# Kernel optimization log

Hardware: AMD Instinct MI355X
Metric: run time of the kernel (lower is better)

The kernel has to match this reference:

```python
import jax, jax.numpy as jnp
import numpy as np

B, IN, OUT, E = 4096, 256, 256, 16


def setup_inputs() -> dict:
    key = jax.random.key(0)
    k1, k2, k3, k4, k5, k6 = jax.random.split(key, 6)
    return {
        "input": jax.random.normal(k1, (B, IN), dtype=jnp.float32),
        "route_index": jax.random.randint(k2, (B,), 0, E),
        "weight": jax.random.normal(k3, (E, OUT * IN), dtype=jnp.float32) * 0.02,
        "weight_fact": jax.random.normal(k4, (1, OUT * IN), dtype=jnp.float32) * 0.02,
        "bias": jax.random.normal(k5, (E, OUT), dtype=jnp.float32) * 0.02,
        "bias_fact": jax.random.normal(k6, (1, OUT), dtype=jnp.float32) * 0.02,
    }


def reference(input, route_index, weight, weight_fact, bias, bias_fact):
    b = input.shape[0]
    # per-token expert weight gather + shared factorized weight
    expert_weight = (weight[route_index] + weight_fact).reshape(b, OUT, IN)
    expert_bias = bias[route_index] + bias_fact  # [b, OUT]
    # batched matvec
    out = jnp.einsum("bmn,bn->bm", expert_weight, input) + expert_bias
    return out
```

## Files before the change

### kernel.cpp

```cpp
#include <hip/hip_runtime.h>


#define B_TOK 4096
#define IN_F 256
#define OUT_F 256
#define NEXP 16
#define WEL (OUT_F * IN_F)
#define NSB 16

typedef __attribute__((ext_vector_type(8))) short bhalf8;
typedef __attribute__((ext_vector_type(4))) float v4f;

__device__ __forceinline__ unsigned short f2bf(float f) {
    unsigned u = __float_as_uint(f);
    u += 0x7FFFu + ((u >> 16) & 1u);
    return (unsigned short)(u >> 16);
}

__device__ __forceinline__ bhalf8 cvt8(float4 a0, float4 a1) {
    bhalf8 v;
    v[0] = (short)f2bf(a0.x); v[1] = (short)f2bf(a0.y);
    v[2] = (short)f2bf(a0.z); v[3] = (short)f2bf(a0.w);
    v[4] = (short)f2bf(a1.x); v[5] = (short)f2bf(a1.y);
    v[6] = (short)f2bf(a1.z); v[7] = (short)f2bf(a1.w);
    return v;
}

__global__ __launch_bounds__(256) void k_fused(
    const float* __restrict__ x, const int* __restrict__ ridx,
    const float* __restrict__ w, const float* __restrict__ wf,
    const float* __restrict__ bias, const float* __restrict__ bfv,
    float* __restrict__ out) {
    __shared__ int pfx[NSB + 1];
    __shared__ int pcs[NSB];
    __shared__ int wc[4];
    __shared__ int stk[16];

    int e = blockIdx.x;
    int j = blockIdx.y;
    int tid = threadIdx.x;
    int wave = tid >> 6;
    int lane = tid & 63;

    {
        int c = 0;
        const int4* rp = (const int4*)(ridx + tid * 16);
        #pragma unroll
        for (int i = 0; i < 4; ++i) {
            int4 v = rp[i];
            c += (v.x == e) + (v.y == e) + (v.z == e) + (v.w == e);
        }
        #pragma unroll
        for (int s = 1; s < 16; s <<= 1) c += __shfl_xor(c, s);
        if ((tid & 15) == 0) pcs[tid >> 4] = c;
    }
    __syncthreads();
    if (tid == 0) {
        int a = 0;
        for (int sb = 0; sb < NSB; ++sb) { pfx[sb] = a; a += pcs[sb]; }
        pfx[NSB] = a;
    }
    __syncthreads();

    int cnt = pfx[NSB];
    int start = j * 16;
    if (start >= cnt) return;
    int rem = cnt - start;
    int rows = rem < 16 ? rem : 16;
    int end = start + rows;

    for (int sb = 0; sb < NSB; ++sb) {
        if (pfx[sb + 1] <= start || pfx[sb] >= end) continue;
        int tok = sb * 256 + tid;
        bool m = (ridx[tok] == e);
        unsigned long long mask = __ballot(m);
        if (lane == 0) wc[wave] = (int)__popcll(mask);
        __syncthreads();
        int wbase = 0;
        for (int wv = 0; wv < wave; ++wv) wbase += wc[wv];
        int rank = wbase + (int)__popcll(mask & ((1ull << lane) - 1ull));
        int slot = pfx[sb] + rank;
        if (m && slot >= start && slot < end) stk[slot - start] = tok;
        __syncthreads();
    }
    if (tid < 16 && tid >= rows) stk[tid] = stk[0];
    __syncthreads();

    int l15 = lane & 15;
    int quad = lane >> 4;

    const float* xrow = x + stk[l15] * IN_F + quad * 8;
    const float* wrow = w + e * WEL + (wave * 64 + l15) * IN_F + quad * 8;
    const float* frow = wf + (wave * 64 + l15) * IN_F + quad * 8;

    v4f acc[4];
    #pragma unroll
    for (int n = 0; n < 4; ++n) acc[n] = (v4f){0.f, 0.f, 0.f, 0.f};

    #pragma unroll
    for (int ks = 0; ks < 8; ++ks) {
        const float4 a0 = *(const float4*)(xrow + ks * 32);
        const float4 a1 = *(const float4*)(xrow + ks * 32 + 4);
        bhalf8 a = cvt8(a0, a1);
        #pragma unroll
        for (int n = 0; n < 4; ++n) {
            const float* wp = wrow + n * (16 * IN_F) + ks * 32;
            const float* fp = frow + n * (16 * IN_F) + ks * 32;
            const float4 b0 = *(const float4*)(wp);
            const float4 b1 = *(const float4*)(wp + 4);
            const float4 g0 = *(const float4*)(fp);
            const float4 g1 = *(const float4*)(fp + 4);
            float4 s0 = make_float4(b0.x + g0.x, b0.y + g0.y,
                                    b0.z + g0.z, b0.w + g0.w);
            float4 s1 = make_float4(b1.x + g1.x, b1.y + g1.y,
                                    b1.z + g1.z, b1.w + g1.w);
            bhalf8 b = cvt8(s0, s1);
            acc[n] = __builtin_amdgcn_mfma_f32_16x16x32_bf16(a, b, acc[n], 0, 0, 0);
        }
    }

    #pragma unroll
    for (int n = 0; n < 4; ++n) {
        int m = wave * 64 + n * 16 + l15;
        float bb = bias[e * OUT_F + m] + bfv[m];
        #pragma unroll
        for (int r = 0; r < 4; ++r) {
            int row = quad * 4 + r;
            if (row < rows) out[stk[row] * OUT_F + m] = acc[n][r] + bb;
        }
    }
}

extern "C" void kernel_launch(void* const* d_in, const int* in_sizes, int n_in,
                              void* d_out, int out_size, void* d_ws, size_t ws_size,
                              hipStream_t stream) {
    (void)in_sizes; (void)n_in; (void)out_size; (void)d_ws; (void)ws_size;
    const float* x = (const float*)d_in[0];
    const int* ridx = (const int*)d_in[1];
    const float* w = (const float*)d_in[2];
    const float* wf = (const float*)d_in[3];
    const float* bias = (const float*)d_in[4];
    const float* bf = (const float*)d_in[5];
    float* out = (float*)d_out;

    k_fused<<<dim3(NEXP, 32), 256, 0, stream>>>(x, ridx, w, wf, bias, bf, out);
}
```

Measured before the change: 101.4 us.

## Precompute bf16 expert weight sums and tile 64 tokens per GEMM block

Adds a pre-pass kernel that adds the shared factor weight to every expert weight once and stores the sum as bf16 in workspace. The GEMM kernel then reads those packed bf16 weights directly. Each block now covers 64 routed tokens instead of 16, so each weight fragment feeds four MFMA token tiles. The aim is to stop re-reading and re-converting the fp32 expert and factor weights in every 16-token block. The cost is an extra launch plus a 2 MB workspace write, and a much smaller gemm grid (16x8) with fewer active blocks.

Measured after the change: 88.90 us. -12.4%, faster.

```diff
diff --git a/kernel.cpp b/kernel.cpp
--- a/kernel.cpp
+++ b/kernel.cpp
@@ -7,9 +7,13 @@
 #define NEXP 16
 #define WEL (OUT_F * IN_F)
 #define NSB 16
+#define TPB 64
+#define JTILES 8
 
 typedef __attribute__((ext_vector_type(8))) short bhalf8;
 typedef __attribute__((ext_vector_type(4))) float v4f;
+
+#define WSUM_OFF 0u
 
 __device__ __forceinline__ unsigned short f2bf(float f) {
     unsigned u = __float_as_uint(f);
@@ -26,15 +30,28 @@
     return v;
 }
 
-__global__ __launch_bounds__(256) void k_fused(
-    const float* __restrict__ x, const int* __restrict__ ridx,
+__global__ __launch_bounds__(256) void k_conv(
     const float* __restrict__ w, const float* __restrict__ wf,
-    const float* __restrict__ bias, const float* __restrict__ bfv,
-    float* __restrict__ out) {
+    unsigned short* __restrict__ wsum) {
+    int id = (blockIdx.x * 256 + threadIdx.x) * 8;
+    const float4 a0 = *(const float4*)(w + id);
+    const float4 a1 = *(const float4*)(w + id + 4);
+    int fo = id & (WEL - 1);
+    const float4 f0 = *(const float4*)(wf + fo);
+    const float4 f1 = *(const float4*)(wf + fo + 4);
+    float4 s0 = make_float4(a0.x + f0.x, a0.y + f0.y, a0.z + f0.z, a0.w + f0.w);
+    float4 s1 = make_float4(a1.x + f1.x, a1.y + f1.y, a1.z + f1.z, a1.w + f1.w);
+    *(bhalf8*)(wsum + id) = cvt8(s0, s1);
+}
+
+__global__ __launch_bounds__(256) void k_gemm(
+    const unsigned short* __restrict__ wsum, const float* __restrict__ x,
+    const int* __restrict__ ridx, const float* __restrict__ bias,
+    const float* __restrict__ bfv, float* __restrict__ out) {
     __shared__ int pfx[NSB + 1];
     __shared__ int pcs[NSB];
     __shared__ int wc[4];
-    __shared__ int stk[16];
+    __shared__ int stk[TPB];
 
     int e = blockIdx.x;
     int j = blockIdx.y;
@@ -63,10 +80,10 @@
     __syncthreads();
 
     int cnt = pfx[NSB];
-    int start = j * 16;
+    int start = j * TPB;
     if (start >= cnt) return;
     int rem = cnt - start;
-    int rows = rem < 16 ? rem : 16;
+    int rows = rem < TPB ? rem : TPB;
     int end = start + rows;
 
     for (int sb = 0; sb < NSB; ++sb) {
@@ -83,50 +100,60 @@
         if (m && slot >= start && slot < end) stk[slot - start] = tok;
         __syncthreads();
     }
-    if (tid < 16 && tid >= rows) stk[tid] = stk[0];
+    if (tid < TPB && tid >= rows) stk[tid] = stk[0];
     __syncthreads();
 
     int l15 = lane & 15;
     int quad = lane >> 4;
 
-    const float* xrow = x + stk[l15] * IN_F + quad * 8;
-    const float* wrow = w + e * WEL + (wave * 64 + l15) * IN_F + quad * 8;
-    const float* frow = wf + (wave * 64 + l15) * IN_F + quad * 8;
+    float bb[4];
+    #pragma unroll
+    for (int n = 0; n < 4; ++n) {
+        int m = wave * 64 + n * 16 + l15;
+        bb[n] = bias[e * OUT_F + m] + bfv[m];
+    }
 
-    v4f acc[4];
+    const unsigned short* wrow =
+        wsum + e * WEL + (wave * 64 + l15) * IN_F + quad * 8;
+    const float* xr[4];
     #pragma unroll
-    for (int n = 0; n < 4; ++n) acc[n] = (v4f){0.f, 0.f, 0.f, 0.f};
+    for (int t = 0; t < 4; ++t)
+        xr[t] = x + stk[t * 16 + l15] * IN_F + quad * 8;
+
+    v4f acc[4][4];
+    #pragma unroll
+    for (int t = 0; t < 4; ++t)
+        #pragma unroll
+        for (int n = 0; n < 4; ++n) acc[t][n] = (v4f){0.f, 0.f, 0.f, 0.f};
 
     #pragma unroll
     for (int ks = 0; ks < 8; ++ks) {
-        const float4 a0 = *(const float4*)(xrow + ks * 32);
-        const float4 a1 = *(const float4*)(xrow + ks * 32 + 4);
-        bhalf8 a = cvt8(a0, a1);
+        bhalf8 b[4];
         #pragma unroll
-        for (int n = 0; n < 4; ++n) {
-            const float* wp = wrow + n * (16 * IN_F) + ks * 32;
-            const float* fp = frow + n * (16 * IN_F) + ks * 32;
-            const float4 b0 = *(const float4*)(wp);
-            const float4 b1 = *(const float4*)(wp + 4);
-            const float4 g0 = *(const float4*)(fp);
-            const float4 g1 = *(const float4*)(fp + 4);
-            float4 s0 = make_float4(b0.x + g0.x, b0.y + g0.y,
-                                    b0.z + g0.z, b0.w + g0.w);
-            float4 s1 = make_float4(b1.x + g1.x, b1.y + g1.y,
-                                    b1.z + g1.z, b1.w + g1.w);
-            bhalf8 b = cvt8(s0, s1);
-            acc[n] = __builtin_amdgcn_mfma_f32_16x16x32_bf16(a, b, acc[n], 0, 0, 0);
+        for (int n = 0; n < 4; ++n)
+            b[n] = *(const bhalf8*)(wrow + n * (16 * IN_F) + ks * 32);
+        #pragma unroll
+        for (int t = 0; t < 4; ++t) {
+            const float4 a0 = *(const float4*)(xr[t] + ks * 32);
+            const float4 a1 = *(const float4*)(xr[t] + ks * 32 + 4);
+            bhalf8 a = cvt8(a0, a1);
+            #pragma unroll
+            for (int n = 0; n < 4; ++n)
+                acc[t][n] =
+                    __builtin_amdgcn_mfma_f32_16x16x32_bf16(a, b[n], acc[t][n], 0, 0, 0);
         }
     }
 
     #pragma unroll
-    for (int n = 0; n < 4; ++n) {
-        int m = wave * 64 + n * 16 + l15;
-        float bb = bias[e * OUT_F + m] + bfv[m];
+    for (int t = 0; t < 4; ++t) {
         #pragma unroll
-        for (int r = 0; r < 4; ++r) {
-            int row = quad * 4 + r;
-            if (row < rows) out[stk[row] * OUT_F + m] = acc[n][r] + bb;
+        for (int n = 0; n < 4; ++n) {
+            int m = wave * 64 + n * 16 + l15;
+            #pragma unroll
+            for (int r = 0; r < 4; ++r) {
+                int rg = t * 16 + quad * 4 + r;
+                if (rg < rows) out[stk[rg] * OUT_F + m] = acc[t][n][r] + bb[n];
+            }
         }
     }
 }
@@ -134,7 +161,7 @@
 extern "C" void kernel_launch(void* const* d_in, const int* in_sizes, int n_in,
                               void* d_out, int out_size, void* d_ws, size_t ws_size,
                               hipStream_t stream) {
-    (void)in_sizes; (void)n_in; (void)out_size; (void)d_ws; (void)ws_size;
+    (void)in_sizes; (void)n_in; (void)out_size; (void)ws_size;
     const float* x = (const float*)d_in[0];
     const int* ridx = (const int*)d_in[1];
     const float* w = (const float*)d_in[2];
@@ -142,6 +169,8 @@
     const float* bias = (const float*)d_in[4];
     const float* bf = (const float*)d_in[5];
     float* out = (float*)d_out;
+    unsigned short* wsum = (unsigned short*)((char*)d_ws + WSUM_OFF);
 
-    k_fused<<<dim3(NEXP, 32), 256, 0, stream>>>(x, ridx, w, wf, bias, bf, out);
+    k_conv<<<512, 256, 0, stream>>>(w, wf, wsum);
+    k_gemm<<<dim3(NEXP, JTILES), 256, 0, stream>>>(wsum, x, ridx, bias, bf, out);
 }
```
